# Performance work log

Measured on AMD Instinct MI355X. Metric: run time of the kernel, lower is better.

## Reference

```python
import jax, jax.numpy as jnp
import numpy as np

IN_FEATURES = 4096
OUT_FEATURES = 14336
GROUP_SIZE = 128  # in_features grouped: 4096 / 128 = 32 groups
N_GROUPS = IN_FEATURES // GROUP_SIZE


def setup_inputs() -> dict:
    key = jax.random.key(0)
    k_x, k_q, k_s, k_zb, k_b = jax.random.split(key, 5)
    x = jax.random.normal(k_x, (8, 32, IN_FEATURES), dtype=jnp.float32)
    # uint8-style affine-quantized weights packed as (in_features, out_features)
    quant_kernel = jax.random.randint(k_q, (IN_FEATURES, OUT_FEATURES), 0, 256, dtype=jnp.int32)
    # per-group scales / zero-point biases: (n_groups, out_features)
    quant_scales = (jax.random.uniform(k_s, (N_GROUPS, OUT_FEATURES), dtype=jnp.float32) + 0.5) * 0.01
    quant_biases = jax.random.normal(k_zb, (N_GROUPS, OUT_FEATURES), dtype=jnp.float32) * 0.01
    bias = jax.random.normal(k_b, (OUT_FEATURES,), dtype=jnp.float32) * 0.02
    return {"x": x, "quant_kernel": quant_kernel, "quant_scales": quant_scales,
            "quant_biases": quant_biases, "bias": bias}


def reference(x, quant_kernel, quant_scales, quant_biases, bias):
    # Affine group-wise dequant: w[f, o] = q[f, o] * scale[f//G, o] + zp_bias[f//G, o]
    q = quant_kernel.astype(jnp.float32).reshape(N_GROUPS, GROUP_SIZE, OUT_FEATURES)
    w = q * quant_scales[:, None, :] + quant_biases[:, None, :]
    w = w.reshape(IN_FEATURES, OUT_FEATURES)
    # y = x @ W + b  (x: [B, S, K], W: [K, N])
    y = jnp.einsum("bsk,kn->bsn", x, w) + bias
    return y
```

## Files before the change

### kernel.cpp

```cpp
#include <hip/hip_runtime.h>
#include <hip/hip_bf16.h>

#define K_DIM 4096
#define N_DIM 14336
#define M_DIM 256
#define BN 64
#define BK 128
#define NITER 32
#define RS 136

typedef __attribute__((ext_vector_type(4))) float f32x4;
typedef __attribute__((ext_vector_type(8))) short short8;

__device__ __forceinline__ unsigned short f2bf(float f) {
    union { float f; unsigned u; } v; v.f = f;
    unsigned r = v.u + 0x7fffu + ((v.u >> 16) & 1u);
    return (unsigned short)(r >> 16);
}

__global__ void convert_x_kernel(const float* __restrict__ x,
                                 unsigned short* __restrict__ xf) {
    int t = blockIdx.x * blockDim.x + threadIdx.x;
    int chunk = t >> 6;
    int lane  = t & 63;
    int ktile = chunk >> 4;
    int mtile = chunk & 15;
    int m = mtile * 16 + (lane & 15);
    int k = ktile * 32 + ((lane >> 4) << 3);
    const float* xp = x + (size_t)m * K_DIM + k;
    float4 lo = *(const float4*)xp;
    float4 hi = *(const float4*)(xp + 4);
    union { unsigned short s[8]; int4 v; } o;
    o.s[0] = f2bf(lo.x); o.s[1] = f2bf(lo.y); o.s[2] = f2bf(lo.z); o.s[3] = f2bf(lo.w);
    o.s[4] = f2bf(hi.x); o.s[5] = f2bf(hi.y); o.s[6] = f2bf(hi.z); o.s[7] = f2bf(hi.w);
    *(int4*)(xf + ((size_t)t << 3)) = o.v;
}

template<bool USE_WS>
__global__ __launch_bounds__(512, 2)
void plq_gemm_kernel(const float* __restrict__ x,
                     const unsigned short* __restrict__ xf,
                     const int* __restrict__ q,
                     const float* __restrict__ qs,
                     const float* __restrict__ qb,
                     const float* __restrict__ bias,
                     float* __restrict__ out)
{
    __shared__ unsigned short wlds[2][BN * RS];

    const int tid  = threadIdx.x;
    const int lane = tid & 63;
    const int wv   = tid >> 6;
    const int wm   = wv >> 1;
    const int wn   = wv & 1;
    const int n0   = blockIdx.x * BN;

    const int tn = tid & 31;
    const int tk = tid >> 5;
    const int nl = tn * 2;
    const int kl = tk * 8;

    f32x4 acc[4][2] = {};

    int2   qr[8];
    float2 sv, zv;

    auto loadq = [&](int i) {
        const int* qp = q + (size_t)(i * BK + kl) * N_DIM + (n0 + nl);
        #pragma unroll
        for (int j = 0; j < 8; ++j)
            qr[j] = *(const int2*)(qp + (size_t)j * N_DIM);
        sv = *(const float2*)(qs + (size_t)i * N_DIM + (n0 + nl));
        zv = *(const float2*)(qb + (size_t)i * N_DIM + (n0 + nl));
    };

    auto deqw = [&](int b) {
        union { unsigned u[4]; int4 v; } p0, p1;
        #pragma unroll
        for (int j = 0; j < 4; ++j) {
            float a0 = (float)qr[2*j].x   * sv.x + zv.x;
            float a1 = (float)qr[2*j+1].x * sv.x + zv.x;
            float c0 = (float)qr[2*j].y   * sv.y + zv.y;
            float c1 = (float)qr[2*j+1].y * sv.y + zv.y;
            p0.u[j] = (unsigned)f2bf(a0) | ((unsigned)f2bf(a1) << 16);
            p1.u[j] = (unsigned)f2bf(c0) | ((unsigned)f2bf(c1) << 16);
        }
        *(int4*)&wlds[b][(nl + 0) * RS + kl] = p0.v;
        *(int4*)&wlds[b][(nl + 1) * RS + kl] = p1.v;
    };

    auto compute = [&](int i, int cur) {
        short8 afr[4][4];
        if (USE_WS) {
            #pragma unroll
            for (int ks = 0; ks < 4; ++ks)
                #pragma unroll
                for (int mf = 0; mf < 4; ++mf) {
                    int chunk = (i * 4 + ks) * 16 + (wm * 4 + mf);
                    afr[ks][mf] = *(const short8*)(xf + ((size_t)chunk << 9) + (size_t)(lane << 3));
                }
        } else {
            #pragma unroll
            for (int ks = 0; ks < 4; ++ks)
                #pragma unroll
                for (int mf = 0; mf < 4; ++mf) {
                    int m = wm * 64 + mf * 16 + (lane & 15);
                    int k = i * BK + ks * 32 + ((lane >> 4) << 3);
                    const float* xp = x + (size_t)m * K_DIM + k;
                    float4 lo = *(const float4*)xp;
                    float4 hi = *(const float4*)(xp + 4);
                    union { unsigned short s[8]; short8 v; } u;
                    u.s[0] = f2bf(lo.x); u.s[1] = f2bf(lo.y); u.s[2] = f2bf(lo.z); u.s[3] = f2bf(lo.w);
                    u.s[4] = f2bf(hi.x); u.s[5] = f2bf(hi.y); u.s[6] = f2bf(hi.z); u.s[7] = f2bf(hi.w);
                    afr[ks][mf] = u.v;
                }
        }
        #pragma unroll
        for (int ks = 0; ks < 4; ++ks) {
            const int kb = ks * 32 + ((lane >> 4) << 3);
            short8 b0 = *(const short8*)&wlds[cur][(wn * 32 +      (lane & 15)) * RS + kb];
            short8 b1 = *(const short8*)&wlds[cur][(wn * 32 + 16 + (lane & 15)) * RS + kb];
            #pragma unroll
            for (int mf = 0; mf < 4; ++mf) {
                acc[mf][0] = __builtin_amdgcn_mfma_f32_16x16x32_bf16(afr[ks][mf], b0, acc[mf][0], 0, 0, 0);
                acc[mf][1] = __builtin_amdgcn_mfma_f32_16x16x32_bf16(afr[ks][mf], b1, acc[mf][1], 0, 0, 0);
            }
        }
    };

    loadq(0);
    deqw(0);
    __syncthreads();

    for (int i = 0; i < NITER; ++i) {
        const int cur = i & 1;
        if (i + 1 < NITER) loadq(i + 1);
        compute(i, cur);
        if (i + 1 < NITER) deqw(cur ^ 1);
        __syncthreads();
    }

    #pragma unroll
    for (int nf = 0; nf < 2; ++nf) {
        const int n = n0 + wn * 32 + nf * 16 + (lane & 15);
        const float bb = bias[n];
        #pragma unroll
        for (int mf = 0; mf < 4; ++mf) {
            const int m0 = wm * 64 + mf * 16 + ((lane >> 4) << 2);
            #pragma unroll
            for (int r = 0; r < 4; ++r)
                out[(size_t)(m0 + r) * N_DIM + n] = acc[mf][nf][r] + bb;
        }
    }
}

extern "C" void kernel_launch(void* const* d_in, const int* in_sizes, int n_in,
                              void* d_out, int out_size, void* d_ws, size_t ws_size,
                              hipStream_t stream) {
    const float* x    = (const float*)d_in[0];
    const int*   qk   = (const int*)d_in[1];
    const float* qs   = (const float*)d_in[2];
    const float* qb   = (const float*)d_in[3];
    const float* bias = (const float*)d_in[4];
    float* out = (float*)d_out;

    const size_t xf_bytes = (size_t)M_DIM * K_DIM * sizeof(unsigned short);
    if (ws_size >= xf_bytes) {
        unsigned short* xf = (unsigned short*)d_ws;
        convert_x_kernel<<<512, 256, 0, stream>>>(x, xf);
        plq_gemm_kernel<true><<<N_DIM / BN, 512, 0, stream>>>(x, xf, qk, qs, qb, bias, out);
    } else {
        plq_gemm_kernel<false><<<N_DIM / BN, 512, 0, stream>>>(x, nullptr, qk, qs, qb, bias, out);
    }
}
```

Baseline: 93.49 us.

## Rewrite GEMM with split-K waves, direct-to-LDS activation loads, and block swizzle

Replaces the workspace GEMM with a new kernel that uses 128-wide N tiles, splits M into halves across blocks and K into halves across waves, and reduces the two K halves through shared memory at the end. Activation tiles are copied straight into LDS with global_load_lds. Quantized weights are double-buffered in registers and dequantized into LDS, with explicit vmcnt waits and barriers. A blockIdx remap groups blocks for cache locality. The aim is better overlap of weight loading with MFMA work and less global traffic for activations, at the cost of more registers, hand-tuned wait counts and an extra reduction step.

```diff
diff --git a/kernel.cpp b/kernel.cpp
--- a/kernel.cpp
+++ b/kernel.cpp
@@ -4,10 +4,10 @@
 #define K_DIM 4096
 #define N_DIM 14336
 #define M_DIM 256
-#define BN 64
-#define BK 128
-#define NITER 32
-#define RS 136
+#define BN 128
+#define BK 32
+#define NIT 64
+#define KHALF 2048
 
 typedef __attribute__((ext_vector_type(4))) float f32x4;
 typedef __attribute__((ext_vector_type(8))) short short8;
@@ -17,6 +17,18 @@
     unsigned r = v.u + 0x7fffu + ((v.u >> 16) & 1u);
     return (unsigned short)(r >> 16);
 }
+
+__device__ __forceinline__ void glds16(const void* g, void* l) {
+    __builtin_amdgcn_global_load_lds(
+        (const __attribute__((address_space(1))) void*)g,
+        (__attribute__((address_space(3))) void*)l, 16, 0, 0);
+}
+
+#define KBAR(N) do { \
+    asm volatile("s_waitcnt vmcnt(" #N ")" ::: "memory"); \
+    asm volatile("s_waitcnt lgkmcnt(0)" ::: "memory");    \
+    __builtin_amdgcn_s_barrier();                          \
+} while (0)
 
 __global__ void convert_x_kernel(const float* __restrict__ x,
                                  unsigned short* __restrict__ xf) {
@@ -36,44 +48,211 @@
     *(int4*)(xf + ((size_t)t << 3)) = o.v;
 }
 
-template<bool USE_WS>
 __global__ __launch_bounds__(512, 2)
-void plq_gemm_kernel(const float* __restrict__ x,
-                     const unsigned short* __restrict__ xf,
-                     const int* __restrict__ q,
-                     const float* __restrict__ qs,
-                     const float* __restrict__ qb,
-                     const float* __restrict__ bias,
-                     float* __restrict__ out)
+void plq_gemm_v6(const unsigned short* __restrict__ xf,
+                 const int* __restrict__ q,
+                 const float* __restrict__ qs,
+                 const float* __restrict__ qb,
+                 const float* __restrict__ bias,
+                 float* __restrict__ out)
 {
-    __shared__ unsigned short wlds[2][BN * RS];
-
+    __shared__ char smem[65536];
+
+    const int tid  = threadIdx.x;
+    const int lane = tid & 63;
+    const int wv   = tid >> 6;
+
+    const int kh = wv & 1;
+    const int wn = (wv >> 1) & 1;
+    const int wm = wv >> 2;
+
+    const int gid = ((blockIdx.x & 7) * 28) + (blockIdx.x >> 3);
+    const int mh  = gid & 1;
+    const int n0  = (gid >> 1) * BN;
+
+    const int n_d  = ((wv & 1) << 6) + lane;
+    const int kh_d = (wv >> 1) & 1;
+    const int g8   = ((wv >> 2) & 1) << 3;
+
+    f32x4 acc[4][4] = {};
+
+    int   qA[16], qB[16];
+    float sA, zA, sB, zB;
+
+    auto issueA = [&](int t, int pb) {
+        #pragma unroll
+        for (int j = 0; j < 2; ++j) {
+            const int flat = (wv << 11) + (j << 10) + (lane << 4);
+            const int kh2  = flat >> 13;
+            const int off  = flat & 8191;
+            const char* src = (const char*)xf
+                + (((size_t)((((kh2 << 6) + t) << 4) + (mh << 3))) << 10) + off;
+            glds16(src, smem + (pb << 14) + flat);
+        }
+    };
+
+    auto issueQA = [&](int t) {
+        const int* base = q + (size_t)(kh_d * KHALF + t * BK) * N_DIM + n0 + n_d;
+        #pragma unroll
+        for (int st = 0; st < 2; ++st)
+            #pragma unroll
+            for (int j = 0; j < 8; ++j)
+                qA[st * 8 + j] = base[(size_t)(g8 + st * 16 + j) * N_DIM];
+        const int g = (kh_d << 4) + (t >> 2);
+        sA = qs[(size_t)g * N_DIM + n0 + n_d];
+        zA = qb[(size_t)g * N_DIM + n0 + n_d];
+    };
+    auto issueQB = [&](int t) {
+        const int* base = q + (size_t)(kh_d * KHALF + t * BK) * N_DIM + n0 + n_d;
+        #pragma unroll
+        for (int st = 0; st < 2; ++st)
+            #pragma unroll
+            for (int j = 0; j < 8; ++j)
+                qB[st * 8 + j] = base[(size_t)(g8 + st * 16 + j) * N_DIM];
+        const int g = (kh_d << 4) + (t >> 2);
+        sB = qs[(size_t)g * N_DIM + n0 + n_d];
+        zB = qb[(size_t)g * N_DIM + n0 + n_d];
+    };
+
+    auto deqA_ = [&](int pb) {
+        char* wbase = smem + 32768 + (pb << 14) + (kh_d << 13) + n_d * 64 + (g8 << 1);
+        #pragma unroll
+        for (int st = 0; st < 2; ++st) {
+            union { unsigned u[4]; int4 v; } pk;
+            #pragma unroll
+            for (int j = 0; j < 4; ++j) {
+                float f0 = (float)qA[st * 8 + 2 * j]     * sA + zA;
+                float f1 = (float)qA[st * 8 + 2 * j + 1] * sA + zA;
+                pk.u[j] = (unsigned)f2bf(f0) | ((unsigned)f2bf(f1) << 16);
+            }
+            *(int4*)(wbase + (st << 5)) = pk.v;
+        }
+    };
+    auto deqB_ = [&](int pb) {
+        char* wbase = smem + 32768 + (pb << 14) + (kh_d << 13) + n_d * 64 + (g8 << 1);
+        #pragma unroll
+        for (int st = 0; st < 2; ++st) {
+            union { unsigned u[4]; int4 v; } pk;
+            #pragma unroll
+            for (int j = 0; j < 4; ++j) {
+                float f0 = (float)qB[st * 8 + 2 * j]     * sB + zB;
+                float f1 = (float)qB[st * 8 + 2 * j + 1] * sB + zB;
+                pk.u[j] = (unsigned)f2bf(f0) | ((unsigned)f2bf(f1) << 16);
+            }
+            *(int4*)(wbase + (st << 5)) = pk.v;
+        }
+    };
+
+    auto compute = [&](int pb) {
+        const char* abase = smem + (pb << 14) + (kh << 13) + (wm << 12) + (lane << 4);
+        const char* bbase = smem + 32768 + (pb << 14) + (kh << 13)
+                          + (((wn << 6) + (lane & 15)) << 6) + ((lane >> 4) << 4);
+        short8 af[4], bf[4];
+        #pragma unroll
+        for (int mf = 0; mf < 4; ++mf)
+            af[mf] = *(const short8*)(abase + (mf << 10));
+        #pragma unroll
+        for (int nf = 0; nf < 4; ++nf)
+            bf[nf] = *(const short8*)(bbase + (nf << 10));
+        #pragma unroll
+        for (int mf = 0; mf < 4; ++mf)
+            #pragma unroll
+            for (int nf = 0; nf < 4; ++nf)
+                acc[mf][nf] = __builtin_amdgcn_mfma_f32_16x16x32_bf16(
+                                  af[mf], bf[nf], acc[mf][nf], 0, 0, 0);
+    };
+
+    issueQA(0);
+    issueQB(1);
+    issueA(0, 0);
+    deqA_(0);
+    KBAR(0);
+
+    #pragma unroll 1
+    for (int ii = 0; ii < 31; ++ii) {
+        const int i = ii << 1;
+
+        issueA(i + 1, 1);
+        issueQA(i + 2);
+        deqB_(1);
+        compute(0);
+        KBAR(18);
+
+        issueA(i + 2, 0);
+        issueQB(i + 3);
+        deqA_(0);
+        compute(1);
+        KBAR(18);
+    }
+    issueA(63, 1);
+    deqB_(1);
+    compute(0);
+    KBAR(0);
+    compute(1);
+    asm volatile("s_waitcnt lgkmcnt(0)" ::: "memory");
+    __builtin_amdgcn_s_barrier();
+
+    if (kh == 1) {
+        char* rb = smem + ((wv >> 1) << 14) + (lane << 4);
+        #pragma unroll
+        for (int mf = 0; mf < 4; ++mf)
+            #pragma unroll
+            for (int nf = 0; nf < 4; ++nf)
+                *(f32x4*)(rb + (((mf << 2) + nf) << 10)) = acc[mf][nf];
+    }
+    asm volatile("s_waitcnt lgkmcnt(0)" ::: "memory");
+    __builtin_amdgcn_s_barrier();
+    if (kh == 0) {
+        const char* rb = smem + ((wv >> 1) << 14) + (lane << 4);
+        #pragma unroll
+        for (int nf = 0; nf < 4; ++nf) {
+            const int n = n0 + (wn << 6) + (nf << 4) + (lane & 15);
+            const float bv = bias[n];
+            #pragma unroll
+            for (int mf = 0; mf < 4; ++mf) {
+                f32x4 o = acc[mf][nf] + *(const f32x4*)(rb + (((mf << 2) + nf) << 10));
+                const int m0 = (mh << 7) + (wm << 6) + (mf << 4) + ((lane >> 4) << 2);
+                #pragma unroll
+                for (int r = 0; r < 4; ++r)
+                    out[(size_t)(m0 + r) * N_DIM + n] = o[r] + bv;
+            }
+        }
+    }
+}
+
+#define FBN 64
+#define FBK 128
+#define FNITER 32
+#define FRS 136
+__global__ __launch_bounds__(512, 2)
+void plq_gemm_fb(const float* __restrict__ x,
+                 const int* __restrict__ q,
+                 const float* __restrict__ qs,
+                 const float* __restrict__ qb,
+                 const float* __restrict__ bias,
+                 float* __restrict__ out)
+{
+    __shared__ unsigned short wlds[2][FBN * FRS];
     const int tid  = threadIdx.x;
     const int lane = tid & 63;
     const int wv   = tid >> 6;
     const int wm   = wv >> 1;
     const int wn   = wv & 1;
-    const int n0   = blockIdx.x * BN;
-
-    const int tn = tid & 31;
-    const int tk = tid >> 5;
-    const int nl = tn * 2;
-    const int kl = tk * 8;
+    const int n0   = blockIdx.x * FBN;
+    const int nl = (tid & 31) * 2;
+    const int kl = (tid >> 5) * 8;
 
     f32x4 acc[4][2] = {};
-
     int2   qr[8];
     float2 sv, zv;
 
     auto loadq = [&](int i) {
-        const int* qp = q + (size_t)(i * BK + kl) * N_DIM + (n0 + nl);
-        #pragma unroll
-        for (int j = 0; j < 8; ++j)
-            qr[j] = *(const int2*)(qp + (size_t)j * N_DIM);
+        const int* qp = q + (size_t)(i * FBK + kl) * N_DIM + (n0 + nl);
+        #pragma unroll
+        for (int j = 0; j < 8; ++j) qr[j] = *(const int2*)(qp + (size_t)j * N_DIM);
         sv = *(const float2*)(qs + (size_t)i * N_DIM + (n0 + nl));
         zv = *(const float2*)(qb + (size_t)i * N_DIM + (n0 + nl));
     };
-
     auto deqw = [&](int b) {
         union { unsigned u[4]; int4 v; } p0, p1;
         #pragma unroll
@@ -85,41 +264,30 @@
             p0.u[j] = (unsigned)f2bf(a0) | ((unsigned)f2bf(a1) << 16);
             p1.u[j] = (unsigned)f2bf(c0) | ((unsigned)f2bf(c1) << 16);
         }
-        *(int4*)&wlds[b][(nl + 0) * RS + kl] = p0.v;
-        *(int4*)&wlds[b][(nl + 1) * RS + kl] = p1.v;
-    };
-
+        *(int4*)&wlds[b][(nl + 0) * FRS + kl] = p0.v;
+        *(int4*)&wlds[b][(nl + 1) * FRS + kl] = p1.v;
+    };
     auto compute = [&](int i, int cur) {
         short8 afr[4][4];
-        if (USE_WS) {
-            #pragma unroll
-            for (int ks = 0; ks < 4; ++ks)
-                #pragma unroll
-                for (int mf = 0; mf < 4; ++mf) {
-                    int chunk = (i * 4 + ks) * 16 + (wm * 4 + mf);
-                    afr[ks][mf] = *(const short8*)(xf + ((size_t)chunk << 9) + (size_t)(lane << 3));
-                }
-        } else {
-            #pragma unroll
-            for (int ks = 0; ks < 4; ++ks)
-                #pragma unroll
-                for (int mf = 0; mf < 4; ++mf) {
-                    int m = wm * 64 + mf * 16 + (lane & 15);
-                    int k = i * BK + ks * 32 + ((lane >> 4) << 3);
-                    const float* xp = x + (size_t)m * K_DIM + k;
-                    float4 lo = *(const float4*)xp;
-                    float4 hi = *(const float4*)(xp + 4);
-                    union { unsigned short s[8]; short8 v; } u;
-                    u.s[0] = f2bf(lo.x); u.s[1] = f2bf(lo.y); u.s[2] = f2bf(lo.z); u.s[3] = f2bf(lo.w);
-                    u.s[4] = f2bf(hi.x); u.s[5] = f2bf(hi.y); u.s[6] = f2bf(hi.z); u.s[7] = f2bf(hi.w);
-                    afr[ks][mf] = u.v;
-                }
-        }
+        #pragma unroll
+        for (int ks = 0; ks < 4; ++ks)
+            #pragma unroll
+            for (int mf = 0; mf < 4; ++mf) {
+                int m = wm * 64 + mf * 16 + (lane & 15);
+                int k = i * FBK + ks * 32 + ((lane >> 4) << 3);
+                const float* xp = x + (size_t)m * K_DIM + k;
+                float4 lo = *(const float4*)xp;
+                float4 hi = *(const float4*)(xp + 4);
+                union { unsigned short s[8]; short8 v; } u;
+                u.s[0] = f2bf(lo.x); u.s[1] = f2bf(lo.y); u.s[2] = f2bf(lo.z); u.s[3] = f2bf(lo.w);
+                u.s[4] = f2bf(hi.x); u.s[5] = f2bf(hi.y); u.s[6] = f2bf(hi.z); u.s[7] = f2bf(hi.w);
+                afr[ks][mf] = u.v;
+            }
         #pragma unroll
         for (int ks = 0; ks < 4; ++ks) {
             const int kb = ks * 32 + ((lane >> 4) << 3);
-            short8 b0 = *(const short8*)&wlds[cur][(wn * 32 +      (lane & 15)) * RS + kb];
-            short8 b1 = *(const short8*)&wlds[cur][(wn * 32 + 16 + (lane & 15)) * RS + kb];
+            short8 b0 = *(const short8*)&wlds[cur][(wn * 32 +      (lane & 15)) * FRS + kb];
+            short8 b1 = *(const short8*)&wlds[cur][(wn * 32 + 16 + (lane & 15)) * FRS + kb];
             #pragma unroll
             for (int mf = 0; mf < 4; ++mf) {
                 acc[mf][0] = __builtin_amdgcn_mfma_f32_16x16x32_bf16(afr[ks][mf], b0, acc[mf][0], 0, 0, 0);
@@ -128,18 +296,14 @@
         }
     };
 
-    loadq(0);
-    deqw(0);
-    __syncthreads();
-
-    for (int i = 0; i < NITER; ++i) {
+    loadq(0); deqw(0); __syncthreads();
+    for (int i = 0; i < FNITER; ++i) {
         const int cur = i & 1;
-        if (i + 1 < NITER) loadq(i + 1);
+        if (i + 1 < FNITER) loadq(i + 1);
         compute(i, cur);
-        if (i + 1 < NITER) deqw(cur ^ 1);
+        if (i + 1 < FNITER) deqw(cur ^ 1);
         __syncthreads();
     }
-
     #pragma unroll
     for (int nf = 0; nf < 2; ++nf) {
         const int n = n0 + wn * 32 + nf * 16 + (lane & 15);
@@ -168,8 +332,8 @@
     if (ws_size >= xf_bytes) {
         unsigned short* xf = (unsigned short*)d_ws;
         convert_x_kernel<<<512, 256, 0, stream>>>(x, xf);
-        plq_gemm_kernel<true><<<N_DIM / BN, 512, 0, stream>>>(x, xf, qk, qs, qb, bias, out);
+        plq_gemm_v6<<<(N_DIM / BN) * 2, 512, 0, stream>>>(xf, qk, qs, qb, bias, out);
     } else {
-        plq_gemm_kernel<false><<<N_DIM / BN, 512, 0, stream>>>(x, nullptr, qk, qs, qb, bias, out);
-    }
-}
+        plq_gemm_fb<<<N_DIM / FBN, 512, 0, stream>>>(x, qk, qs, qb, bias, out);
+    }
+}
```

Result: slower. 99.65 us (+6.6%).

## Split M into four tiles with XCD-aware block mapping and register double-buffered weight pipeline

Applied to the files above, without the earlier changes.

Replaces the 224-block GEMM with 896 smaller 256-thread blocks, each computing a 64x64 output tile. The intent is to fill all compute units instead of leaving some idle. Block IDs are remapped so the four M-tiles sharing one weight column strip run on the same XCD, so repeated reads of the quantized weights can hit in L2. The K step is halved, and weights are fetched into two alternating register sets with explicit vmcnt waits, so global loads, dequantization and MFMA work overlap. The trade-off is that each weight strip is dequantized four times and more scale/bias loads are issued.

```diff
diff --git a/kernel.cpp b/kernel.cpp
--- a/kernel.cpp
+++ b/kernel.cpp
@@ -4,10 +4,11 @@
 #define K_DIM 4096
 #define N_DIM 14336
 #define M_DIM 256
+#define BM 64
 #define BN 64
-#define BK 128
-#define NITER 32
-#define RS 136
+#define BK 64
+#define NPH 64
+#define RS 72
 
 typedef __attribute__((ext_vector_type(4))) float f32x4;
 typedef __attribute__((ext_vector_type(8))) short short8;
@@ -17,6 +18,12 @@
     unsigned r = v.u + 0x7fffu + ((v.u >> 16) & 1u);
     return (unsigned short)(r >> 16);
 }
+
+#define KBAR(N) do { \
+    asm volatile("s_waitcnt lgkmcnt(0)" ::: "memory");     \
+    asm volatile("s_waitcnt vmcnt(" #N ")" ::: "memory");  \
+    __builtin_amdgcn_s_barrier();                           \
+} while (0)
 
 __global__ void convert_x_kernel(const float* __restrict__ x,
                                  unsigned short* __restrict__ xf) {
@@ -36,44 +43,180 @@
     *(int4*)(xf + ((size_t)t << 3)) = o.v;
 }
 
-template<bool USE_WS>
-__global__ __launch_bounds__(512, 2)
-void plq_gemm_kernel(const float* __restrict__ x,
-                     const unsigned short* __restrict__ xf,
-                     const int* __restrict__ q,
-                     const float* __restrict__ qs,
-                     const float* __restrict__ qb,
-                     const float* __restrict__ bias,
-                     float* __restrict__ out)
+__global__ __launch_bounds__(256, 4)
+void plq_gemm_v8(const unsigned short* __restrict__ xf,
+                 const int* __restrict__ q,
+                 const float* __restrict__ qs,
+                 const float* __restrict__ qb,
+                 const float* __restrict__ bias,
+                 float* __restrict__ out)
 {
-    __shared__ unsigned short wlds[2][BN * RS];
+    __shared__ unsigned short w0[BN * RS];
+    __shared__ unsigned short w1[BN * RS];
 
     const int tid  = threadIdx.x;
     const int lane = tid & 63;
     const int wv   = tid >> 6;
     const int wm   = wv >> 1;
     const int wn   = wv & 1;
-    const int n0   = blockIdx.x * BN;
-
-    const int tn = tid & 31;
-    const int tk = tid >> 5;
-    const int nl = tn * 2;
-    const int kl = tk * 8;
+
+    const int gid = (blockIdx.x & 7) * 112 + (blockIdx.x >> 3);
+    const int mt  = gid & 3;
+    const int n0  = (gid >> 2) * BN;
+
+    const int qn   = tid & 63;
+    const int qk0  = (tid >> 6) << 4;
+    const size_t qcol = (size_t)n0 + qn;
+
+    f32x4 acc[2][2] = {};
+    short8 af[2][2];
+    int   qA[16], qB[16];
+    float sA, zA, sB, zB;
+
+    auto issueQA = [&](int t) {
+        const int* p = q + (size_t)(t * BK + qk0) * N_DIM + qcol;
+        #pragma unroll
+        for (int j = 0; j < 16; ++j) qA[j] = p[(size_t)j * N_DIM];
+        const int g = t >> 1;
+        sA = qs[(size_t)g * N_DIM + qcol];
+        zA = qb[(size_t)g * N_DIM + qcol];
+    };
+    auto issueQB = [&](int t) {
+        const int* p = q + (size_t)(t * BK + qk0) * N_DIM + qcol;
+        #pragma unroll
+        for (int j = 0; j < 16; ++j) qB[j] = p[(size_t)j * N_DIM];
+        const int g = t >> 1;
+        sB = qs[(size_t)g * N_DIM + qcol];
+        zB = qb[(size_t)g * N_DIM + qcol];
+    };
+    auto deqA = [&](unsigned short* dst) {
+        union { unsigned u[4]; int4 v; } p0, p1;
+        #pragma unroll
+        for (int j = 0; j < 4; ++j) {
+            float f0 = (float)qA[2*j]     * sA + zA;
+            float f1 = (float)qA[2*j+1]   * sA + zA;
+            float f2 = (float)qA[8+2*j]   * sA + zA;
+            float f3 = (float)qA[8+2*j+1] * sA + zA;
+            p0.u[j] = (unsigned)f2bf(f0) | ((unsigned)f2bf(f1) << 16);
+            p1.u[j] = (unsigned)f2bf(f2) | ((unsigned)f2bf(f3) << 16);
+        }
+        *(int4*)&dst[qn * RS + qk0]     = p0.v;
+        *(int4*)&dst[qn * RS + qk0 + 8] = p1.v;
+    };
+    auto deqB = [&](unsigned short* dst) {
+        union { unsigned u[4]; int4 v; } p0, p1;
+        #pragma unroll
+        for (int j = 0; j < 4; ++j) {
+            float f0 = (float)qB[2*j]     * sB + zB;
+            float f1 = (float)qB[2*j+1]   * sB + zB;
+            float f2 = (float)qB[8+2*j]   * sB + zB;
+            float f3 = (float)qB[8+2*j+1] * sB + zB;
+            p0.u[j] = (unsigned)f2bf(f0) | ((unsigned)f2bf(f1) << 16);
+            p1.u[j] = (unsigned)f2bf(f2) | ((unsigned)f2bf(f3) << 16);
+        }
+        *(int4*)&dst[qn * RS + qk0]     = p0.v;
+        *(int4*)&dst[qn * RS + qk0 + 8] = p1.v;
+    };
+    auto loadAfr = [&](int i) {
+        #pragma unroll
+        for (int ks = 0; ks < 2; ++ks)
+            #pragma unroll
+            for (int mf = 0; mf < 2; ++mf) {
+                const int ktile = i * 2 + ks;
+                const int mtile = mt * 4 + wm * 2 + mf;
+                af[ks][mf] = *(const short8*)(xf
+                    + ((size_t)(ktile * 16 + mtile) << 9) + (lane << 3));
+            }
+    };
+    auto mfma = [&](const unsigned short* buf) {
+        #pragma unroll
+        for (int ks = 0; ks < 2; ++ks) {
+            const int kb = ks * 32 + ((lane >> 4) << 3);
+            short8 b0 = *(const short8*)&buf[(wn * 32 +      (lane & 15)) * RS + kb];
+            short8 b1 = *(const short8*)&buf[(wn * 32 + 16 + (lane & 15)) * RS + kb];
+            acc[0][0] = __builtin_amdgcn_mfma_f32_16x16x32_bf16(af[ks][0], b0, acc[0][0], 0, 0, 0);
+            acc[0][1] = __builtin_amdgcn_mfma_f32_16x16x32_bf16(af[ks][0], b1, acc[0][1], 0, 0, 0);
+            acc[1][0] = __builtin_amdgcn_mfma_f32_16x16x32_bf16(af[ks][1], b0, acc[1][0], 0, 0, 0);
+            acc[1][1] = __builtin_amdgcn_mfma_f32_16x16x32_bf16(af[ks][1], b1, acc[1][1], 0, 0, 0);
+        }
+    };
+
+    issueQA(0);
+    issueQB(1);
+    deqA(w0);
+    KBAR(18);
+
+    #pragma unroll 1
+    for (int ii = 0; ii < 31; ++ii) {
+        const int i = ii << 1;
+
+        loadAfr(i);
+        issueQA(i + 2);
+        deqB(w1);
+        mfma(w0);
+        KBAR(18);
+
+        loadAfr(i + 1);
+        issueQB(i + 3);
+        deqA(w0);
+        mfma(w1);
+        KBAR(18);
+    }
+
+    loadAfr(62);
+    deqB(w1);
+    mfma(w0);
+    KBAR(0);
+    loadAfr(63);
+    mfma(w1);
+
+    #pragma unroll
+    for (int nf = 0; nf < 2; ++nf) {
+        const int n = n0 + wn * 32 + nf * 16 + (lane & 15);
+        const float bv = bias[n];
+        #pragma unroll
+        for (int mf = 0; mf < 2; ++mf) {
+            const int m0 = mt * 64 + wm * 32 + mf * 16 + ((lane >> 4) << 2);
+            #pragma unroll
+            for (int r = 0; r < 4; ++r)
+                out[(size_t)(m0 + r) * N_DIM + n] = acc[mf][nf][r] + bv;
+        }
+    }
+}
+
+#define FBN 64
+#define FBK 128
+#define FNITER 32
+#define FRS 136
+__global__ __launch_bounds__(512, 2)
+void plq_gemm_fb(const float* __restrict__ x,
+                 const int* __restrict__ q,
+                 const float* __restrict__ qs,
+                 const float* __restrict__ qb,
+                 const float* __restrict__ bias,
+                 float* __restrict__ out)
+{
+    __shared__ unsigned short wlds[2][FBN * FRS];
+    const int tid  = threadIdx.x;
+    const int lane = tid & 63;
+    const int wv   = tid >> 6;
+    const int wm   = wv >> 1;
+    const int wn   = wv & 1;
+    const int n0   = blockIdx.x * FBN;
+    const int nl = (tid & 31) * 2;
+    const int kl = (tid >> 5) * 8;
 
     f32x4 acc[4][2] = {};
-
     int2   qr[8];
     float2 sv, zv;
 
     auto loadq = [&](int i) {
-        const int* qp = q + (size_t)(i * BK + kl) * N_DIM + (n0 + nl);
-        #pragma unroll
-        for (int j = 0; j < 8; ++j)
-            qr[j] = *(const int2*)(qp + (size_t)j * N_DIM);
+        const int* qp = q + (size_t)(i * FBK + kl) * N_DIM + (n0 + nl);
+        #pragma unroll
+        for (int j = 0; j < 8; ++j) qr[j] = *(const int2*)(qp + (size_t)j * N_DIM);
         sv = *(const float2*)(qs + (size_t)i * N_DIM + (n0 + nl));
         zv = *(const float2*)(qb + (size_t)i * N_DIM + (n0 + nl));
     };
-
     auto deqw = [&](int b) {
         union { unsigned u[4]; int4 v; } p0, p1;
         #pragma unroll
@@ -85,41 +228,30 @@
             p0.u[j] = (unsigned)f2bf(a0) | ((unsigned)f2bf(a1) << 16);
             p1.u[j] = (unsigned)f2bf(c0) | ((unsigned)f2bf(c1) << 16);
         }
-        *(int4*)&wlds[b][(nl + 0) * RS + kl] = p0.v;
-        *(int4*)&wlds[b][(nl + 1) * RS + kl] = p1.v;
-    };
-
+        *(int4*)&wlds[b][(nl + 0) * FRS + kl] = p0.v;
+        *(int4*)&wlds[b][(nl + 1) * FRS + kl] = p1.v;
+    };
     auto compute = [&](int i, int cur) {
         short8 afr[4][4];
-        if (USE_WS) {
-            #pragma unroll
-            for (int ks = 0; ks < 4; ++ks)
-                #pragma unroll
-                for (int mf = 0; mf < 4; ++mf) {
-                    int chunk = (i * 4 + ks) * 16 + (wm * 4 + mf);
-                    afr[ks][mf] = *(const short8*)(xf + ((size_t)chunk << 9) + (size_t)(lane << 3));
-                }
-        } else {
-            #pragma unroll
-            for (int ks = 0; ks < 4; ++ks)
-                #pragma unroll
-                for (int mf = 0; mf < 4; ++mf) {
-                    int m = wm * 64 + mf * 16 + (lane & 15);
-                    int k = i * BK + ks * 32 + ((lane >> 4) << 3);
-                    const float* xp = x + (size_t)m * K_DIM + k;
-                    float4 lo = *(const float4*)xp;
-                    float4 hi = *(const float4*)(xp + 4);
-                    union { unsigned short s[8]; short8 v; } u;
-                    u.s[0] = f2bf(lo.x); u.s[1] = f2bf(lo.y); u.s[2] = f2bf(lo.z); u.s[3] = f2bf(lo.w);
-                    u.s[4] = f2bf(hi.x); u.s[5] = f2bf(hi.y); u.s[6] = f2bf(hi.z); u.s[7] = f2bf(hi.w);
-                    afr[ks][mf] = u.v;
-                }
-        }
+        #pragma unroll
+        for (int ks = 0; ks < 4; ++ks)
+            #pragma unroll
+            for (int mf = 0; mf < 4; ++mf) {
+                int m = wm * 64 + mf * 16 + (lane & 15);
+                int k = i * FBK + ks * 32 + ((lane >> 4) << 3);
+                const float* xp = x + (size_t)m * K_DIM + k;
+                float4 lo = *(const float4*)xp;
+                float4 hi = *(const float4*)(xp + 4);
+                union { unsigned short s[8]; short8 v; } u;
+                u.s[0] = f2bf(lo.x); u.s[1] = f2bf(lo.y); u.s[2] = f2bf(lo.z); u.s[3] = f2bf(lo.w);
+                u.s[4] = f2bf(hi.x); u.s[5] = f2bf(hi.y); u.s[6] = f2bf(hi.z); u.s[7] = f2bf(hi.w);
+                afr[ks][mf] = u.v;
+            }
         #pragma unroll
         for (int ks = 0; ks < 4; ++ks) {
             const int kb = ks * 32 + ((lane >> 4) << 3);
-            short8 b0 = *(const short8*)&wlds[cur][(wn * 32 +      (lane & 15)) * RS + kb];
-            short8 b1 = *(const short8*)&wlds[cur][(wn * 32 + 16 + (lane & 15)) * RS + kb];
+            short8 b0 = *(const short8*)&wlds[cur][(wn * 32 +      (lane & 15)) * FRS + kb];
+            short8 b1 = *(const short8*)&wlds[cur][(wn * 32 + 16 + (lane & 15)) * FRS + kb];
             #pragma unroll
             for (int mf = 0; mf < 4; ++mf) {
                 acc[mf][0] = __builtin_amdgcn_mfma_f32_16x16x32_bf16(afr[ks][mf], b0, acc[mf][0], 0, 0, 0);
@@ -128,18 +260,14 @@
         }
     };
 
-    loadq(0);
-    deqw(0);
-    __syncthreads();
-
-    for (int i = 0; i < NITER; ++i) {
+    loadq(0); deqw(0); __syncthreads();
+    for (int i = 0; i < FNITER; ++i) {
         const int cur = i & 1;
-        if (i + 1 < NITER) loadq(i + 1);
+        if (i + 1 < FNITER) loadq(i + 1);
         compute(i, cur);
-        if (i + 1 < NITER) deqw(cur ^ 1);
+        if (i + 1 < FNITER) deqw(cur ^ 1);
         __syncthreads();
     }
-
     #pragma unroll
     for (int nf = 0; nf < 2; ++nf) {
         const int n = n0 + wn * 32 + nf * 16 + (lane & 15);
@@ -168,8 +296,9 @@
     if (ws_size >= xf_bytes) {
         unsigned short* xf = (unsigned short*)d_ws;
         convert_x_kernel<<<512, 256, 0, stream>>>(x, xf);
-        plq_gemm_kernel<true><<<N_DIM / BN, 512, 0, stream>>>(x, xf, qk, qs, qb, bias, out);
+        const int grid = (M_DIM / BM) * (N_DIM / BN);
+        plq_gemm_v8<<<grid, 256, 0, stream>>>(xf, qk, qs, qb, bias, out);
     } else {
-        plq_gemm_kernel<false><<<N_DIM / BN, 512, 0, stream>>>(x, nullptr, qk, qs, qb, bias, out);
-    }
-}
+        plq_gemm_fb<<<N_DIM / FBN, 512, 0, stream>>>(x, qk, qs, qb, bias, out);
+    }
+}
```

Result: slower. 118.6 us (+26.8%).
